# Kernel tuning notes

Hardware: AMD Instinct MI355X
Metric: run time of the kernel (lower is better)

Reference implementation:

```python
import jax, jax.numpy as jnp
import numpy as np

_EPS = 1e-12  # torch F.normalize eps


def _normalize(x):
    # x: [B, N, 3]; matches torch.nn.functional.normalize(x, dim=2)
    norm = jnp.linalg.norm(x, axis=2, keepdims=True)
    return x / jnp.maximum(norm, _EPS)


def setup_inputs() -> dict:
    key = jax.random.key(0)
    k1, k2 = jax.random.split(key)
    xyz1 = jax.random.normal(k1, (8, 4096, 6), dtype=jnp.float32)
    xyz2 = jax.random.normal(k2, (8, 4096, 6), dtype=jnp.float32)
    return {"xyz1": xyz1, "xyz2": xyz2}


def reference(xyz1, xyz2):
    p1 = xyz1[:, :, :3]  # [B, N, 3]
    p2 = xyz2[:, :, :3]  # [B, M, 3]
    n1 = xyz1[:, :, 3:]  # [B, N, 3]
    n2 = xyz2[:, :, 3:]  # [B, M, 3]

    # Pairwise squared L2: |a|^2 + |b|^2 - 2 a.b  -> [B, N, M]
    sq1 = jnp.sum(p1 * p1, axis=2)  # [B, N]
    sq2 = jnp.sum(p2 * p2, axis=2)  # [B, M]
    cross = jnp.einsum('bnd,bmd->bnm', p1, p2)
    d = sq1[:, :, None] + sq2[:, None, :] - 2.0 * cross  # [B, N, M]

    dist1 = jnp.min(d, axis=2)      # [B, N] NN of each p1 in p2
    idx1 = jnp.argmin(d, axis=2)    # [B, N]
    dist2 = jnp.min(d, axis=1)      # [B, M] NN of each p2 in p1
    idx2 = jnp.argmin(d, axis=1)    # [B, M]

    # Gather matched normals
    t1 = jnp.take_along_axis(n2, idx1[:, :, None], axis=1)  # [B, N, 3]
    t2 = jnp.take_along_axis(n1, idx2[:, :, None], axis=1)  # [B, M, 3]

    nd1 = jnp.sum((_normalize(n1) - _normalize(t1)) ** 2, axis=2)  # [B, N]
    nd2 = jnp.sum((_normalize(n2) - _normalize(t2)) ** 2, axis=2)  # [B, M]

    return jnp.mean(dist1) + jnp.mean(dist2) + jnp.mean(nd1) + jnp.mean(nd2)
```

## Files before the change

### kernel.cpp

```cpp
#include <hip/hip_runtime.h>
#include <cstdint>

#define NB 8
#define NP 4096
#define THREADS 256
#define Q 4
#define CHUNK (THREADS * Q)
#define NCHUNK (NP / CHUNK)


template <int SEGV>
__global__ __launch_bounds__(THREADS) void chamfer_argmin(
    const float* __restrict__ xyz1, const float* __restrict__ xyz2,
    unsigned int* __restrict__ part)
{
    const int TSEG = NP / SEGV;
    __shared__ float4 tgt[NP / 16];

    unsigned int x = blockIdx.x;
    int seg   = x & (SEGV - 1);
    int chunk = (x / SEGV) & (NCHUNK - 1);
    int b     = (x / (SEGV * NCHUNK)) & 7;
    int dir   = x / (SEGV * NCHUNK * 8);

    const float* qset = dir ? xyz2 : xyz1;
    const float* tset = dir ? xyz1 : xyz2;

    int tbase = seg * TSEG;
    for (int t0 = threadIdx.x; t0 < TSEG; t0 += THREADS) {
        const float* src = tset + ((size_t)b * NP + tbase + t0) * 6;
        float tx = src[0], ty = src[1], tz = src[2];
        tgt[t0] = make_float4(tx, ty, tz, -0.5f * (tx * tx + ty * ty + tz * tz));
    }
    __syncthreads();

    float qx[Q], qy[Q], qz[Q], qq[Q], bs[Q];
    unsigned int bi[Q];
    int qbase = chunk * CHUNK + threadIdx.x;
    #pragma unroll
    for (int i = 0; i < Q; ++i) {
        const float* src = qset + ((size_t)b * NP + qbase + i * THREADS) * 6;
        qx[i] = src[0]; qy[i] = src[1]; qz[i] = src[2];
        qq[i] = qx[i] * qx[i] + qy[i] * qy[i] + qz[i] * qz[i];
        bs[i] = -3.4e38f;
        bi[i] = 0u;
    }

    #pragma unroll 4
    for (int k = 0; k < TSEG; ++k) {
        float4 t = tgt[k];
        unsigned int jb = (unsigned int)(tbase + k);
        #pragma unroll
        for (int i = 0; i < Q; ++i) {
            float s = fmaf(t.x, qx[i], fmaf(t.y, qy[i], fmaf(t.z, qz[i], t.w)));
            if (s > bs[i]) { bs[i] = s; bi[i] = jb; }
        }
    }

    unsigned int* slot =
        part + (((size_t)(dir * NB + b) * SEGV + seg) * NP) + qbase;
    #pragma unroll
    for (int i = 0; i < Q; ++i) {
        float d = fmaxf(fmaf(-2.0f, bs[i], qq[i]), 0.0f);
        slot[i * THREADS] = (__float_as_uint(d) & 0xFFFFF000u) | bi[i];
    }
}

template <int SEGV>
__global__ __launch_bounds__(256) void chamfer_finish(
    const float* __restrict__ xyz1, const float* __restrict__ xyz2,
    const unsigned int* __restrict__ part, float* __restrict__ out)
{
    int gid = blockIdx.x * 256 + threadIdx.x;
    int q   = gid & (NP - 1);
    int db  = gid >> 12;
    int b   = db & 7;
    int dir = db >> 3;

    const unsigned int* base = part + ((size_t)db * SEGV) * NP + q;
    unsigned int p = 0xFFFFFFFFu;
    #pragma unroll
    for (int s = 0; s < SEGV; ++s) p = min(p, base[(size_t)s * NP]);

    const float* qset = dir ? xyz2 : xyz1;
    const float* tset = dir ? xyz1 : xyz2;

    float dist = __uint_as_float(p & 0xFFFFF000u);
    int j = (int)(p & 0xFFFu);

    const float* nq = qset + ((size_t)b * NP + q) * 6 + 3;
    const float* nt = tset + ((size_t)b * NP + j) * 6 + 3;
    float ax = nq[0], ay = nq[1], az = nq[2];
    float bx = nt[0], by = nt[1], bz = nt[2];

    float na = fmaxf(sqrtf(ax * ax + ay * ay + az * az), 1e-12f);
    float nb = fmaxf(sqrtf(bx * bx + by * by + bz * bz), 1e-12f);
    float ra = 1.0f / na, rb = 1.0f / nb;
    float dx = ax * ra - bx * rb;
    float dy = ay * ra - by * rb;
    float dz = az * ra - bz * rb;
    float nd = dx * dx + dy * dy + dz * dz;

    float contrib = (dist + nd) * (1.0f / 32768.0f);

    for (int off = 32; off > 0; off >>= 1)
        contrib += __shfl_down(contrib, off, 64);
    __shared__ float wsum[4];
    if ((threadIdx.x & 63) == 0) wsum[threadIdx.x >> 6] = contrib;
    __syncthreads();
    if (threadIdx.x == 0)
        atomicAdd(out, wsum[0] + wsum[1] + wsum[2] + wsum[3]);
}

extern "C" void kernel_launch(void* const* d_in, const int* in_sizes, int n_in,
                              void* d_out, int out_size, void* d_ws, size_t ws_size,
                              hipStream_t stream) {
    const float* xyz1 = (const float*)d_in[0];
    const float* xyz2 = (const float*)d_in[1];
    float* out = (float*)d_out;
    unsigned int* part = (unsigned int*)d_ws;

    hipMemsetAsync(d_out, 0, sizeof(float), stream);

    size_t need32 = (size_t)2 * NB * 32 * NP * sizeof(unsigned int);
    if (ws_size >= need32) {
        chamfer_argmin<32><<<2 * NB * NCHUNK * 32, THREADS, 0, stream>>>(xyz1, xyz2, part);
        chamfer_finish<32><<<(2 * NB * NP) / 256, 256, 0, stream>>>(xyz1, xyz2, part, out);
    } else {
        chamfer_argmin<16><<<2 * NB * NCHUNK * 16, THREADS, 0, stream>>>(xyz1, xyz2, part);
        chamfer_finish<16><<<(2 * NB * NP) / 256, 256, 0, stream>>>(xyz1, xyz2, part, out);
    }
}
```

Before: 94.29 us.

## Fuse argmin and finish kernels with last-block reduction, raise queries per thread

Merges the two kernels into one. Each block computes the normal-difference term for its own per-segment candidate and stores it next to the packed distance/index key. The last block per (direction,batch), found with an atomic counter, reduces across segments, and a second counter lets the last of those write the final sum. Queries per thread rise from 4 to 8, halving chunks, so there are 1024 blocks instead of 2048. The select becomes branchless. The cost is a serial tail: only 16 blocks do the segment reduction, and every block now does redundant normal math and gathers for candidates that will be discarded.

```diff
diff --git a/kernel.cpp b/kernel.cpp
--- a/kernel.cpp
+++ b/kernel.cpp
@@ -3,34 +3,44 @@
 
 #define NB 8
 #define NP 4096
+#define NDB 16
 #define THREADS 256
-#define Q 4
+#define Q 8
 #define CHUNK (THREADS * Q)
 #define NCHUNK (NP / CHUNK)
+#define SEG 32
+#define TSEG (NP / SEG)
+#define BPD (NCHUNK * SEG)
 
 
-template <int SEGV>
-__global__ __launch_bounds__(THREADS) void chamfer_argmin(
+__global__ __launch_bounds__(THREADS) void chamfer_fused(
     const float* __restrict__ xyz1, const float* __restrict__ xyz2,
-    unsigned int* __restrict__ part)
+    unsigned int* __restrict__ ws, float* __restrict__ out)
 {
-    const int TSEG = NP / SEGV;
-    __shared__ float4 tgt[NP / 16];
+    unsigned int* cnt   = ws;
+    unsigned int* gcnt  = ws + 16;
+    float*        dbsum = (float*)(ws + 32);
+    unsigned int* keys  = ws + 1024;
+    float*        nds   = (float*)(ws + 1024 + NDB * SEG * NP);
+
+    __shared__ float4 tgt[TSEG];
 
     unsigned int x = blockIdx.x;
-    int seg   = x & (SEGV - 1);
-    int chunk = (x / SEGV) & (NCHUNK - 1);
-    int b     = (x / (SEGV * NCHUNK)) & 7;
-    int dir   = x / (SEGV * NCHUNK * 8);
+    int seg   = x & (SEG - 1);
+    int chunk = (x >> 5) & (NCHUNK - 1);
+    int db    = x >> 6;
+    int b     = db & 7;
+    int dir   = db >> 3;
 
     const float* qset = dir ? xyz2 : xyz1;
     const float* tset = dir ? xyz1 : xyz2;
 
     int tbase = seg * TSEG;
-    for (int t0 = threadIdx.x; t0 < TSEG; t0 += THREADS) {
-        const float* src = tset + ((size_t)b * NP + tbase + t0) * 6;
+    if (threadIdx.x < TSEG) {
+        const float* src = tset + ((size_t)b * NP + tbase + threadIdx.x) * 6;
         float tx = src[0], ty = src[1], tz = src[2];
-        tgt[t0] = make_float4(tx, ty, tz, -0.5f * (tx * tx + ty * ty + tz * tz));
+        tgt[threadIdx.x] =
+            make_float4(tx, ty, tz, -0.5f * (tx * tx + ty * ty + tz * tz));
     }
     __syncthreads();
 
@@ -53,63 +63,74 @@
         #pragma unroll
         for (int i = 0; i < Q; ++i) {
             float s = fmaf(t.x, qx[i], fmaf(t.y, qy[i], fmaf(t.z, qz[i], t.w)));
-            if (s > bs[i]) { bs[i] = s; bi[i] = jb; }
+            bi[i] = (s > bs[i]) ? jb : bi[i];
+            bs[i] = fmaxf(bs[i], s);
         }
     }
 
-    unsigned int* slot =
-        part + (((size_t)(dir * NB + b) * SEGV + seg) * NP) + qbase;
+    size_t srow = ((size_t)db * SEG + seg) * NP;
     #pragma unroll
     for (int i = 0; i < Q; ++i) {
+        int q = qbase + i * THREADS;
+        int j = (int)bi[i];
         float d = fmaxf(fmaf(-2.0f, bs[i], qq[i]), 0.0f);
-        slot[i * THREADS] = (__float_as_uint(d) & 0xFFFFF000u) | bi[i];
+        unsigned int key = (__float_as_uint(d) & 0xFFFFF000u) | (unsigned int)j;
+
+        const float* nq = qset + ((size_t)b * NP + q) * 6 + 3;
+        const float* nt = tset + ((size_t)b * NP + j) * 6 + 3;
+        float ax = nq[0], ay = nq[1], az = nq[2];
+        float bx = nt[0], by = nt[1], bz = nt[2];
+        float na = fmaxf(sqrtf(ax * ax + ay * ay + az * az), 1e-12f);
+        float nbv = fmaxf(sqrtf(bx * bx + by * by + bz * bz), 1e-12f);
+        float ra = 1.0f / na, rb = 1.0f / nbv;
+        float dx = ax * ra - bx * rb;
+        float dy = ay * ra - by * rb;
+        float dz = az * ra - bz * rb;
+        float nd = dx * dx + dy * dy + dz * dz;
+
+        keys[srow + q] = key;
+        nds[srow + q]  = nd;
     }
-}
 
-template <int SEGV>
-__global__ __launch_bounds__(256) void chamfer_finish(
-    const float* __restrict__ xyz1, const float* __restrict__ xyz2,
-    const unsigned int* __restrict__ part, float* __restrict__ out)
-{
-    int gid = blockIdx.x * 256 + threadIdx.x;
-    int q   = gid & (NP - 1);
-    int db  = gid >> 12;
-    int b   = db & 7;
-    int dir = db >> 3;
+    __threadfence();
+    __syncthreads();
+    __shared__ unsigned int done;
+    if (threadIdx.x == 0) done = atomicAdd(&cnt[db], 1u);
+    __syncthreads();
+    if (done != BPD - 1) return;
 
-    const unsigned int* base = part + ((size_t)db * SEGV) * NP + q;
-    unsigned int p = 0xFFFFFFFFu;
-    #pragma unroll
-    for (int s = 0; s < SEGV; ++s) p = min(p, base[(size_t)s * NP]);
+    __threadfence();
+    const unsigned int* kb = keys + (size_t)db * SEG * NP;
+    const float*        nb = nds + (size_t)db * SEG * NP;
+    float acc = 0.0f;
+    for (int q = threadIdx.x; q < NP; q += THREADS) {
+        unsigned int p = kb[q];
+        int wseg = 0;
+        #pragma unroll
+        for (int s2 = 1; s2 < SEG; ++s2) {
+            unsigned int v = kb[(size_t)s2 * NP + q];
+            if (v < p) { p = v; wseg = s2; }
+        }
+        float dist = __uint_as_float(p & 0xFFFFF000u);
+        acc += dist + nb[(size_t)wseg * NP + q];
+    }
+    for (int off = 32; off > 0; off >>= 1)
+        acc += __shfl_down(acc, off, 64);
+    __shared__ float wsum[4];
+    if ((threadIdx.x & 63) == 0) wsum[threadIdx.x >> 6] = acc;
+    __syncthreads();
+    if (threadIdx.x != 0) return;
 
-    const float* qset = dir ? xyz2 : xyz1;
-    const float* tset = dir ? xyz1 : xyz2;
-
-    float dist = __uint_as_float(p & 0xFFFFF000u);
-    int j = (int)(p & 0xFFFu);
-
-    const float* nq = qset + ((size_t)b * NP + q) * 6 + 3;
-    const float* nt = tset + ((size_t)b * NP + j) * 6 + 3;
-    float ax = nq[0], ay = nq[1], az = nq[2];
-    float bx = nt[0], by = nt[1], bz = nt[2];
-
-    float na = fmaxf(sqrtf(ax * ax + ay * ay + az * az), 1e-12f);
-    float nb = fmaxf(sqrtf(bx * bx + by * by + bz * bz), 1e-12f);
-    float ra = 1.0f / na, rb = 1.0f / nb;
-    float dx = ax * ra - bx * rb;
-    float dy = ay * ra - by * rb;
-    float dz = az * ra - bz * rb;
-    float nd = dx * dx + dy * dy + dz * dz;
-
-    float contrib = (dist + nd) * (1.0f / 32768.0f);
-
-    for (int off = 32; off > 0; off >>= 1)
-        contrib += __shfl_down(contrib, off, 64);
-    __shared__ float wsum[4];
-    if ((threadIdx.x & 63) == 0) wsum[threadIdx.x >> 6] = contrib;
-    __syncthreads();
-    if (threadIdx.x == 0)
-        atomicAdd(out, wsum[0] + wsum[1] + wsum[2] + wsum[3]);
+    dbsum[db] = (wsum[0] + wsum[1] + wsum[2] + wsum[3]) * (1.0f / 32768.0f);
+    __threadfence();
+    unsigned int o2 = atomicAdd(gcnt, 1u);
+    if (o2 == NDB - 1) {
+        __threadfence();
+        float t = 0.0f;
+        #pragma unroll
+        for (int k2 = 0; k2 < NDB; ++k2) t += dbsum[k2];
+        *out = t;
+    }
 }
 
 extern "C" void kernel_launch(void* const* d_in, const int* in_sizes, int n_in,
@@ -117,17 +138,9 @@
                               hipStream_t stream) {
     const float* xyz1 = (const float*)d_in[0];
     const float* xyz2 = (const float*)d_in[1];
-    float* out = (float*)d_out;
-    unsigned int* part = (unsigned int*)d_ws;
 
-    hipMemsetAsync(d_out, 0, sizeof(float), stream);
+    hipMemsetAsync(d_ws, 0, 68, stream);
 
-    size_t need32 = (size_t)2 * NB * 32 * NP * sizeof(unsigned int);
-    if (ws_size >= need32) {
-        chamfer_argmin<32><<<2 * NB * NCHUNK * 32, THREADS, 0, stream>>>(xyz1, xyz2, part);
-        chamfer_finish<32><<<(2 * NB * NP) / 256, 256, 0, stream>>>(xyz1, xyz2, part, out);
-    } else {
-        chamfer_argmin<16><<<2 * NB * NCHUNK * 16, THREADS, 0, stream>>>(xyz1, xyz2, part);
-        chamfer_finish<16><<<(2 * NB * NP) / 256, 256, 0, stream>>>(xyz1, xyz2, part, out);
-    }
+    chamfer_fused<<<NDB * BPD, THREADS, 0, stream>>>(
+        xyz1, xyz2, (unsigned int*)d_ws, (float*)d_out);
 }
```

Result: slower. 219.6 us (+133.0%).
